# Kernel tuning notes

Measured on AMD Instinct MI355X. Metric: run time of the kernel, lower is better.

Reference implementation:

```python
import jax, jax.numpy as jnp
import numpy as np

_SIGMA = 1.5
_K1 = 0.01
_K2 = 0.03
_WINDOW_SIZE = 11
_N_CHANNELS = 3
_VALUE_RANGE = 1.0
_WEIGHTS = np.array([0.0448, 0.2856, 0.3001, 0.2363, 0.1333], dtype=np.float32)


def create_window(window_size: int, n_channels: int) -> jnp.ndarray:
    # 2D Gaussian kernel, normalized to sum 1, expanded to depthwise (C,1,ws,ws)
    coords = np.arange(window_size, dtype=np.float32) - (window_size - 1) / 2.0
    g = np.exp(-(coords ** 2) / (2.0 * _SIGMA ** 2))
    g = g / g.sum()
    k2d = np.outer(g, g).astype(np.float32)  # (ws, ws), sums to 1
    window = np.broadcast_to(k2d[None, None], (n_channels, 1, window_size, window_size))
    return jnp.asarray(window)


def _dwconv(x, window):
    # depthwise valid conv, NCHW / OIHW
    c = x.shape[1]
    return jax.lax.conv_general_dilated(
        x, window, window_strides=(1, 1), padding='VALID',
        dimension_numbers=('NCHW', 'OIHW', 'NCHW'), feature_group_count=c)


def _avg_pool2(x):
    # torch F.avg_pool2d(kernel=2, stride=2, padding=(H%2, W%2), count_include_pad=True)
    ph = x.shape[-2] % 2
    pw = x.shape[-1] % 2
    s = jax.lax.reduce_window(
        x, 0.0, jax.lax.add, window_dimensions=(1, 1, 2, 2),
        window_strides=(1, 1, 2, 2), padding=((0, 0), (0, 0), (ph, ph), (pw, pw)))
    return s * 0.25


def ssim_per_channel(x, y, window, value_range):
    mu_x = _dwconv(x, window)
    mu_y = _dwconv(y, window)
    mu_x_sq = mu_x ** 2
    mu_y_sq = mu_y ** 2
    mu_xy = mu_x * mu_y
    sigma_x_sq = _dwconv(x * x, window) - mu_x_sq
    sigma_y_sq = _dwconv(y * y, window) - mu_y_sq
    sigma_xy = _dwconv(x * y, window) - mu_xy
    c1 = (_K1 * value_range) ** 2
    c2 = (_K2 * value_range) ** 2
    cs_map = (2.0 * sigma_xy + c2) / (sigma_x_sq + sigma_y_sq + c2)
    ssim_map = (2.0 * mu_xy + c1) / (mu_x_sq + mu_y_sq + c1) * cs_map
    return ssim_map.mean(axis=(-1, -2)), cs_map.mean(axis=(-1, -2))  # (N, C) each


def msssim_per_channel(x, y, window, weights, value_range):
    n_scales = weights.shape[0]
    mcs = []
    for i in range(n_scales):
        if i > 0:
            x = _avg_pool2(x)
            y = _avg_pool2(y)
        ssim_val, cs = ssim_per_channel(x, y, window, value_range)
        mcs.append(jax.nn.relu(cs))
    stacked = jnp.stack(mcs[:-1] + [ssim_val], axis=0)  # (M, N, C)
    stacked = stacked ** weights[:, None, None]
    return jnp.prod(stacked, axis=0)  # (N, C)


def setup_inputs() -> dict:
    key = jax.random.key(0)
    k1, k2 = jax.random.split(key)
    N, C, H, W = 16, 3, 512, 512
    x = jax.random.uniform(k1, (N, C, H, W), dtype=jnp.float32)
    # target correlated with input (realistic distorted-image pair)
    noise = jax.random.uniform(k2, (N, C, H, W), dtype=jnp.float32)
    y = jnp.clip(0.9 * x + 0.1 * noise, 0.0, 1.0)
    window = create_window(_WINDOW_SIZE, _N_CHANNELS)
    weights = jnp.asarray(_WEIGHTS)
    return {"x": x, "y": y, "window": window, "weights": weights}


def reference(x, y, window, weights):
    l = msssim_per_channel(x, y, window, weights, _VALUE_RANGE).mean(axis=-1)  # (N,)
    return l.mean()  # reduction='mean' -> scalar
```

## Files before the change

kernel.cpp:

```cpp
#include <hip/hip_runtime.h>

#define HALO 10
#define NPAIR 76

typedef float v2f __attribute__((ext_vector_type(2)));

#define G0 0.00102838f
#define G1 0.00759871f
#define G2 0.03600077f
#define G3 0.10936069f
#define G4 0.21300556f
#define G5 0.26601176f
#define G6 G4
#define G7 G3
#define G8 G2
#define G9 G1
#define G10 G0

#define HTAP(Q, GW)  { hm += (Q) * (GW); hs += ((Q) * (Q)) * (GW); }

__global__ __launch_bounds__(256, 3) void ssim_wave_kernel(
    const float* __restrict__ x, const float* __restrict__ y,
    float* __restrict__ xo, float* __restrict__ yo,
    float* __restrict__ acc, int H, int W, int ROWS, int do_pool)
{
    const int OH = H - HALO, OW = W - HALO;
    const int nc = blockIdx.z;
    const int tid = threadIdx.x;
    const int wave = tid >> 6, lane = tid & 63;
    const int col0 = blockIdx.x * 64;
    const int r0 = (blockIdx.y * 4 + wave) * ROWS;

    const int c = col0 + lane;
    const bool colvalid = (c < OW);
    const int cl = min(c, W - 1);
    const int chalo = min(col0 + 64 + lane, W - 1);

    const int n_out = min(ROWS, OH - r0);
    const int poolrows = do_pool ? min(ROWS, H - r0) : 0;
    const int n_iter = max(n_out > 0 ? n_out + HALO : 0, poolrows);

    const float* xp = x + (size_t)nc * H * W;
    const float* yp = y + (size_t)nc * H * W;

    __shared__ v2f sUD[4][NPAIR];
    v2f* myUD = sUD[wave];

    v2f Hm0={0.f,0.f}, Hm1=Hm0, Hm2=Hm0, Hm3=Hm0, Hm4=Hm0, Hm5=Hm0,
        Hm6=Hm0, Hm7=Hm0, Hm8=Hm0, Hm9=Hm0, Hm10=Hm0;
    v2f Hs0=Hm0, Hs1=Hm0, Hs2=Hm0, Hs3=Hm0, Hs4=Hm0, Hs5=Hm0,
        Hs6=Hm0, Hs7=Hm0, Hs8=Hm0, Hs9=Hm0, Hs10=Hm0;

    float ssim_sum = 0.f, cs_sum = 0.f;

    float ax = 0.f, ay = 0.f, ahx = 0.f, ahy = 0.f;
    float bx = 0.f, by = 0.f, bhx = 0.f, bhy = 0.f;
    float prevx = 0.f, prevy = 0.f;

    const int Wo = W >> 1;
    float* xop = xo + (size_t)nc * (H >> 1) * Wo + (col0 >> 1);
    float* yop = yo + (size_t)nc * (H >> 1) * Wo + (col0 >> 1);
    const int par = lane & 1;

    if (n_iter > 0) {
        {
            const float* rx = xp + (size_t)r0 * W;
            const float* ry = yp + (size_t)r0 * W;
            ax = rx[cl]; ay = ry[cl];
            if (lane < HALO) { ahx = rx[chalo]; ahy = ry[chalo]; }
            const int r1 = min(r0 + 1, H - 1);
            const float* rx1 = xp + (size_t)r1 * W;
            const float* ry1 = yp + (size_t)r1 * W;
            bx = rx1[cl]; by = ry1[cl];
            if (lane < HALO) { bhx = rx1[chalo]; bhy = ry1[chalo]; }
        }
        const int NI = ((n_iter + 10) / 11) * 11;
        for (int ii = 0; ii < NI; ii += 11) {
#pragma unroll
            for (int u = 0; u < 11; ++u) {
                const int i = ii + u;

                if (do_pool && i < poolrows) {
                    float sx2 = ax + __shfl_xor(ax, 1, 64);
                    float sy2 = ay + __shfl_xor(ay, 1, 64);
                    if (i & 1) {
                        if (par == 0) {
                            const int pr = (r0 + i) >> 1;
                            xop[(size_t)pr * Wo + (lane >> 1)] = 0.25f * (prevx + sx2);
                            yop[(size_t)pr * Wo + (lane >> 1)] = 0.25f * (prevy + sy2);
                        }
                    } else { prevx = sx2; prevy = sy2; }
                }

                {
                    v2f ud; ud.x = ax + ay; ud.y = ax - ay;
                    myUD[lane] = ud;
                    if (lane < HALO) {
                        v2f hh; hh.x = ahx + ahy; hh.y = ahx - ahy;
                        myUD[64 + lane] = hh;
                    }
                }

                {
                    const int rr = min(r0 + i + 2, H - 1);
                    const float* rx = xp + (size_t)rr * W;
                    const float* ry = yp + (size_t)rr * W;
                    ax = rx[cl]; ay = ry[cl];
                    if (lane < HALO) { ahx = rx[chalo]; ahy = ry[chalo]; }
                }

                const v2f* pq = myUD + lane;
                const v2f q0 = pq[0], q1 = pq[1], q2 = pq[2], q3 = pq[3],
                          q4 = pq[4], q5 = pq[5], q6 = pq[6], q7 = pq[7],
                          q8 = pq[8], q9 = pq[9], q10 = pq[10];
                v2f hm = {0.f, 0.f}, hs = {0.f, 0.f};
                HTAP(q0, G0)  HTAP(q1, G1)  HTAP(q2, G2)  HTAP(q3, G3)
                HTAP(q4, G4)  HTAP(q5, G5)  HTAP(q6, G6)  HTAP(q7, G7)
                HTAP(q8, G8)  HTAP(q9, G9)  HTAP(q10, G10)

                Hm0=Hm1; Hm1=Hm2; Hm2=Hm3; Hm3=Hm4; Hm4=Hm5; Hm5=Hm6;
                Hm6=Hm7; Hm7=Hm8; Hm8=Hm9; Hm9=Hm10; Hm10=hm;
                Hs0=Hs1; Hs1=Hs2; Hs2=Hs3; Hs3=Hs4; Hs4=Hs5; Hs5=Hs6;
                Hs6=Hs7; Hs7=Hs8; Hs8=Hs9; Hs9=Hs10; Hs10=hs;

                const int o = i - HALO;
                if (o >= 0 && o < n_out && colvalid) {
                    v2f vm = Hm0*G0; vm += Hm1*G1; vm += Hm2*G2; vm += Hm3*G3;
                    vm += Hm4*G4; vm += Hm5*G5; vm += Hm6*G6; vm += Hm7*G7;
                    vm += Hm8*G8; vm += Hm9*G9; vm += Hm10*G10;
                    v2f vs = Hs0*G0; vs += Hs1*G1; vs += Hs2*G2; vs += Hs3*G3;
                    vs += Hs4*G4; vs += Hs5*G5; vs += Hs6*G6; vs += Hs7*G7;
                    vs += Hs8*G8; vs += Hs9*G9; vs += Hs10*G10;

                    const float A = vm.x, B = vm.y;
                    const float a2 = A * A, b2 = B * B;
                    const float mu_xy = 0.25f * (a2 - b2);
                    const float msum  = 0.5f  * (a2 + b2);
                    const float sig_s  = 0.5f  * (vs.x + vs.y) - msum;
                    const float sig_xy = 0.25f * (vs.x - vs.y) - mu_xy;
                    const float c1 = 1e-4f, c2 = 9e-4f;
                    const float cs = (2.f * sig_xy + c2) * __builtin_amdgcn_rcpf(sig_s + c2);
                    const float ssim = (2.f * mu_xy + c1) * __builtin_amdgcn_rcpf(msum + c1) * cs;
                    ssim_sum += ssim;
                    cs_sum += cs;
                }

                {
                    float t;
                    t = ax;  ax = bx;   bx = t;
                    t = ay;  ay = by;   by = t;
                    t = ahx; ahx = bhx; bhx = t;
                    t = ahy; ahy = bhy; bhy = t;
                }
            }
        }
    }

#pragma unroll
    for (int off = 32; off > 0; off >>= 1) {
        ssim_sum += __shfl_down(ssim_sum, off, 64);
        cs_sum   += __shfl_down(cs_sum,   off, 64);
    }
    if (lane == 0) {
        atomicAdd(&acc[nc * 2 + 0], ssim_sum);
        atomicAdd(&acc[nc * 2 + 1], cs_sum);
    }
}

__global__ void finalize_kernel(const float* __restrict__ acc,
                                const float* __restrict__ weights,
                                float* __restrict__ out)
{
    int t = threadIdx.x;
    float v = 0.f;
    if (t < 48) {
        float prod = 1.f;
#pragma unroll
        for (int s = 0; s < 5; ++s) {
            int O = (512 >> s) - HALO;
            float inv = 1.f / ((float)O * (float)O);
            float ssim = acc[s * 96 + t * 2 + 0] * inv;
            float cs   = acc[s * 96 + t * 2 + 1] * inv;
            float val = (s < 4) ? fmaxf(cs, 0.f) : ssim;
            prod *= powf(val, weights[s]);
        }
        v = prod;
    }
#pragma unroll
    for (int off = 32; off > 0; off >>= 1) v += __shfl_down(v, off, 64);
    if (t == 0) out[0] = v * (1.f / 48.f);
}

extern "C" void kernel_launch(void* const* d_in, const int* in_sizes, int n_in,
                              void* d_out, int out_size, void* d_ws, size_t ws_size,
                              hipStream_t stream) {
    const float* x = (const float*)d_in[0];
    const float* y = (const float*)d_in[1];
    const float* weights = (const float*)d_in[3];
    float* out = (float*)d_out;
    float* ws = (float*)d_ws;

    float* acc = ws;
    float* xs1 = ws + 512;
    float* ys1 = xs1 + (size_t)48 * 256 * 256;
    float* xs2 = ys1 + (size_t)48 * 256 * 256;
    float* ys2 = xs2 + (size_t)48 * 128 * 128;
    float* xs3 = ys2 + (size_t)48 * 128 * 128;
    float* ys3 = xs3 + (size_t)48 * 64 * 64;
    float* xs4 = ys3 + (size_t)48 * 64 * 64;
    float* ys4 = xs4 + (size_t)48 * 32 * 32;

    hipMemsetAsync(acc, 0, 480 * sizeof(float), stream);

    dim3 blk(256);
    ssim_wave_kernel<<<dim3(8, 2, 48), blk, 0, stream>>>(x, y, xs1, ys1, acc + 0 * 96, 512, 512, 64, 1);
    ssim_wave_kernel<<<dim3(4, 2, 48), blk, 0, stream>>>(xs1, ys1, xs2, ys2, acc + 1 * 96, 256, 256, 32, 1);
    ssim_wave_kernel<<<dim3(2, 2, 48), blk, 0, stream>>>(xs2, ys2, xs3, ys3, acc + 2 * 96, 128, 128, 16, 1);
    ssim_wave_kernel<<<dim3(1, 2, 48), blk, 0, stream>>>(xs3, ys3, xs4, ys4, acc + 3 * 96, 64, 64, 8, 1);
    ssim_wave_kernel<<<dim3(1, 1, 48), blk, 0, stream>>>(xs4, ys4, nullptr, nullptr, acc + 4 * 96, 32, 32, 8, 0);

    finalize_kernel<<<dim3(1), dim3(64), 0, stream>>>(acc, weights, out);
}
```

Measured before the change: 256.9 us.

## Double-buffer LDS row staging, prefetch three rows ahead, retune per-scale grid splits

The per-wave LDS row buffer is split into two alternating buffers. Each iteration now reads the previous row's taps before writing the next row, which removes the write-then-read dependency within an iteration, and global loads are issued three rows ahead instead of two. The loop is unrolled by 12, matching a three-register rotation, and exits early instead of running padded iterations. The rows-per-wave and grid shapes for scales 2, 4 and 5 are also retuned. In exchange, LDS use doubles and register pressure rises, and the changed row splits alter the halo-recompute overhead and the number of blocks.

```diff
diff --git a/kernel.cpp b/kernel.cpp
--- a/kernel.cpp
+++ b/kernel.cpp
@@ -19,6 +19,76 @@
 
 #define HTAP(Q, GW)  { hm += (Q) * (GW); hs += ((Q) * (Q)) * (GW); }
 
+
+#define LOADROW(RR, AX, AY, HX, HY)                                  \
+    { const float* rx_ = xp + (size_t)(RR) * W;                      \
+      const float* ry_ = yp + (size_t)(RR) * W;                      \
+      AX = rx_[cl]; AY = ry_[cl];                                    \
+      if (lane < HALO) { HX = rx_[chalo]; HY = ry_[chalo]; } }
+
+#define ITER(U, PAX, PAY, PHX, PHY, SAX, SAY, SHX, SHY)              \
+  {                                                                  \
+    const int i = ii + (U);                                          \
+    if (i >= n_iter) break;                                          \
+     \
+    const v2f* pq = (((U) & 1) ? sB : sA) + lane;                    \
+    const v2f q0 = pq[0], q1 = pq[1], q2 = pq[2], q3 = pq[3],        \
+              q4 = pq[4], q5 = pq[5], q6 = pq[6], q7 = pq[7],        \
+              q8 = pq[8], q9 = pq[9], q10 = pq[10];                  \
+            \
+    if (do_pool && i < poolrows) {                                   \
+        float sx2 = PAX + __shfl_xor(PAX, 1, 64);                    \
+        float sy2 = PAY + __shfl_xor(PAY, 1, 64);                    \
+        if (i & 1) {                                                 \
+            if (par == 0) {                                          \
+                const int pr = (r0 + i) >> 1;                        \
+                xop[(size_t)pr * Wo + (lane >> 1)] = 0.25f * (prevx + sx2); \
+                yop[(size_t)pr * Wo + (lane >> 1)] = 0.25f * (prevy + sy2); \
+            }                                                        \
+        } else { prevx = sx2; prevy = sy2; }                         \
+    }                                                                \
+      \
+    { v2f ud_; ud_.x = SAX + SAY; ud_.y = SAX - SAY;                 \
+      (((U) & 1) ? sA : sB)[lane] = ud_;                             \
+      if (lane < HALO) {                                             \
+          v2f hh_; hh_.x = SHX + SHY; hh_.y = SHX - SHY;             \
+          (((U) & 1) ? sA : sB)[64 + lane] = hh_; } }                \
+          \
+    { const int rr_ = min(r0 + i + 3, H - 1);                        \
+      LOADROW(rr_, PAX, PAY, PHX, PHY) }                             \
+                    \
+    v2f hm = {0.f, 0.f}, hs = {0.f, 0.f};                            \
+    HTAP(q0, G0)  HTAP(q1, G1)  HTAP(q2, G2)  HTAP(q3, G3)           \
+    HTAP(q4, G4)  HTAP(q5, G5)  HTAP(q6, G6)  HTAP(q7, G7)           \
+    HTAP(q8, G8)  HTAP(q9, G9)  HTAP(q10, G10)                       \
+     \
+    Hm0=Hm1; Hm1=Hm2; Hm2=Hm3; Hm3=Hm4; Hm4=Hm5; Hm5=Hm6;           \
+    Hm6=Hm7; Hm7=Hm8; Hm8=Hm9; Hm9=Hm10; Hm10=hm;                   \
+    Hs0=Hs1; Hs1=Hs2; Hs2=Hs3; Hs3=Hs4; Hs4=Hs5; Hs5=Hs6;           \
+    Hs6=Hs7; Hs7=Hs8; Hs8=Hs9; Hs9=Hs10; Hs10=hs;                   \
+                                         \
+    const int o = i - HALO;                                          \
+    if (o >= 0 && o < n_out && colvalid) {                           \
+        v2f vm = Hm0*G0; vm += Hm1*G1; vm += Hm2*G2; vm += Hm3*G3;   \
+        vm += Hm4*G4; vm += Hm5*G5; vm += Hm6*G6; vm += Hm7*G7;      \
+        vm += Hm8*G8; vm += Hm9*G9; vm += Hm10*G10;                  \
+        v2f vs = Hs0*G0; vs += Hs1*G1; vs += Hs2*G2; vs += Hs3*G3;   \
+        vs += Hs4*G4; vs += Hs5*G5; vs += Hs6*G6; vs += Hs7*G7;      \
+        vs += Hs8*G8; vs += Hs9*G9; vs += Hs10*G10;                  \
+        const float A = vm.x, B = vm.y;                              \
+        const float a2 = A * A, b2 = B * B;                          \
+        const float mu_xy = 0.25f * (a2 - b2);                       \
+        const float msum  = 0.5f  * (a2 + b2);                       \
+        const float sig_s  = 0.5f  * (vs.x + vs.y) - msum;           \
+        const float sig_xy = 0.25f * (vs.x - vs.y) - mu_xy;          \
+        const float c1 = 1e-4f, c2 = 9e-4f;                          \
+        const float cs = (2.f * sig_xy + c2) * __builtin_amdgcn_rcpf(sig_s + c2); \
+        const float ssim = (2.f * mu_xy + c1) * __builtin_amdgcn_rcpf(msum + c1) * cs; \
+        ssim_sum += ssim;                                            \
+        cs_sum += cs;                                                \
+    }                                                                \
+  }
+
 __global__ __launch_bounds__(256, 3) void ssim_wave_kernel(
     const float* __restrict__ x, const float* __restrict__ y,
     float* __restrict__ xo, float* __restrict__ yo,
@@ -43,8 +113,9 @@
     const float* xp = x + (size_t)nc * H * W;
     const float* yp = y + (size_t)nc * H * W;
 
-    __shared__ v2f sUD[4][NPAIR];
-    v2f* myUD = sUD[wave];
+    __shared__ v2f sUD[4][2][NPAIR];
+    v2f* sA = sUD[wave][0];
+    v2f* sB = sUD[wave][1];
 
     v2f Hm0={0.f,0.f}, Hm1=Hm0, Hm2=Hm0, Hm3=Hm0, Hm4=Hm0, Hm5=Hm0,
         Hm6=Hm0, Hm7=Hm0, Hm8=Hm0, Hm9=Hm0, Hm10=Hm0;
@@ -53,8 +124,9 @@
 
     float ssim_sum = 0.f, cs_sum = 0.f;
 
-    float ax = 0.f, ay = 0.f, ahx = 0.f, ahy = 0.f;
-    float bx = 0.f, by = 0.f, bhx = 0.f, bhy = 0.f;
+    float ax0=0.f, ay0=0.f, ahx0=0.f, ahy0=0.f;
+    float ax1=0.f, ay1=0.f, ahx1=0.f, ahy1=0.f;
+    float ax2=0.f, ay2=0.f, ahx2=0.f, ahy2=0.f;
     float prevx = 0.f, prevy = 0.f;
 
     const int Wo = W >> 1;
@@ -63,96 +135,27 @@
     const int par = lane & 1;
 
     if (n_iter > 0) {
-        {
-            const float* rx = xp + (size_t)r0 * W;
-            const float* ry = yp + (size_t)r0 * W;
-            ax = rx[cl]; ay = ry[cl];
-            if (lane < HALO) { ahx = rx[chalo]; ahy = ry[chalo]; }
-            const int r1 = min(r0 + 1, H - 1);
-            const float* rx1 = xp + (size_t)r1 * W;
-            const float* ry1 = yp + (size_t)r1 * W;
-            bx = rx1[cl]; by = ry1[cl];
-            if (lane < HALO) { bhx = rx1[chalo]; bhy = ry1[chalo]; }
-        }
-        const int NI = ((n_iter + 10) / 11) * 11;
-        for (int ii = 0; ii < NI; ii += 11) {
-#pragma unroll
-            for (int u = 0; u < 11; ++u) {
-                const int i = ii + u;
-
-                if (do_pool && i < poolrows) {
-                    float sx2 = ax + __shfl_xor(ax, 1, 64);
-                    float sy2 = ay + __shfl_xor(ay, 1, 64);
-                    if (i & 1) {
-                        if (par == 0) {
-                            const int pr = (r0 + i) >> 1;
-                            xop[(size_t)pr * Wo + (lane >> 1)] = 0.25f * (prevx + sx2);
-                            yop[(size_t)pr * Wo + (lane >> 1)] = 0.25f * (prevy + sy2);
-                        }
-                    } else { prevx = sx2; prevy = sy2; }
-                }
-
-                {
-                    v2f ud; ud.x = ax + ay; ud.y = ax - ay;
-                    myUD[lane] = ud;
-                    if (lane < HALO) {
-                        v2f hh; hh.x = ahx + ahy; hh.y = ahx - ahy;
-                        myUD[64 + lane] = hh;
-                    }
-                }
-
-                {
-                    const int rr = min(r0 + i + 2, H - 1);
-                    const float* rx = xp + (size_t)rr * W;
-                    const float* ry = yp + (size_t)rr * W;
-                    ax = rx[cl]; ay = ry[cl];
-                    if (lane < HALO) { ahx = rx[chalo]; ahy = ry[chalo]; }
-                }
-
-                const v2f* pq = myUD + lane;
-                const v2f q0 = pq[0], q1 = pq[1], q2 = pq[2], q3 = pq[3],
-                          q4 = pq[4], q5 = pq[5], q6 = pq[6], q7 = pq[7],
-                          q8 = pq[8], q9 = pq[9], q10 = pq[10];
-                v2f hm = {0.f, 0.f}, hs = {0.f, 0.f};
-                HTAP(q0, G0)  HTAP(q1, G1)  HTAP(q2, G2)  HTAP(q3, G3)
-                HTAP(q4, G4)  HTAP(q5, G5)  HTAP(q6, G6)  HTAP(q7, G7)
-                HTAP(q8, G8)  HTAP(q9, G9)  HTAP(q10, G10)
-
-                Hm0=Hm1; Hm1=Hm2; Hm2=Hm3; Hm3=Hm4; Hm4=Hm5; Hm5=Hm6;
-                Hm6=Hm7; Hm7=Hm8; Hm8=Hm9; Hm9=Hm10; Hm10=hm;
-                Hs0=Hs1; Hs1=Hs2; Hs2=Hs3; Hs3=Hs4; Hs4=Hs5; Hs5=Hs6;
-                Hs6=Hs7; Hs7=Hs8; Hs8=Hs9; Hs9=Hs10; Hs10=hs;
-
-                const int o = i - HALO;
-                if (o >= 0 && o < n_out && colvalid) {
-                    v2f vm = Hm0*G0; vm += Hm1*G1; vm += Hm2*G2; vm += Hm3*G3;
-                    vm += Hm4*G4; vm += Hm5*G5; vm += Hm6*G6; vm += Hm7*G7;
-                    vm += Hm8*G8; vm += Hm9*G9; vm += Hm10*G10;
-                    v2f vs = Hs0*G0; vs += Hs1*G1; vs += Hs2*G2; vs += Hs3*G3;
-                    vs += Hs4*G4; vs += Hs5*G5; vs += Hs6*G6; vs += Hs7*G7;
-                    vs += Hs8*G8; vs += Hs9*G9; vs += Hs10*G10;
-
-                    const float A = vm.x, B = vm.y;
-                    const float a2 = A * A, b2 = B * B;
-                    const float mu_xy = 0.25f * (a2 - b2);
-                    const float msum  = 0.5f  * (a2 + b2);
-                    const float sig_s  = 0.5f  * (vs.x + vs.y) - msum;
-                    const float sig_xy = 0.25f * (vs.x - vs.y) - mu_xy;
-                    const float c1 = 1e-4f, c2 = 9e-4f;
-                    const float cs = (2.f * sig_xy + c2) * __builtin_amdgcn_rcpf(sig_s + c2);
-                    const float ssim = (2.f * mu_xy + c1) * __builtin_amdgcn_rcpf(msum + c1) * cs;
-                    ssim_sum += ssim;
-                    cs_sum += cs;
-                }
-
-                {
-                    float t;
-                    t = ax;  ax = bx;   bx = t;
-                    t = ay;  ay = by;   by = t;
-                    t = ahx; ahx = bhx; bhx = t;
-                    t = ahy; ahy = bhy; bhy = t;
-                }
-            }
+        LOADROW(r0, ax0, ay0, ahx0, ahy0)
+        { const int r1_ = min(r0 + 1, H - 1); LOADROW(r1_, ax1, ay1, ahx1, ahy1) }
+        { const int r2_ = min(r0 + 2, H - 1); LOADROW(r2_, ax2, ay2, ahx2, ahy2) }
+        { v2f ud_; ud_.x = ax0 + ay0; ud_.y = ax0 - ay0; sA[lane] = ud_;
+          if (lane < HALO) {
+              v2f hh_; hh_.x = ahx0 + ahy0; hh_.y = ahx0 - ahy0;
+              sA[64 + lane] = hh_; } }
+
+        for (int ii = 0; ii < n_iter; ii += 12) {
+            ITER(0,  ax0, ay0, ahx0, ahy0,  ax1, ay1, ahx1, ahy1)
+            ITER(1,  ax1, ay1, ahx1, ahy1,  ax2, ay2, ahx2, ahy2)
+            ITER(2,  ax2, ay2, ahx2, ahy2,  ax0, ay0, ahx0, ahy0)
+            ITER(3,  ax0, ay0, ahx0, ahy0,  ax1, ay1, ahx1, ahy1)
+            ITER(4,  ax1, ay1, ahx1, ahy1,  ax2, ay2, ahx2, ahy2)
+            ITER(5,  ax2, ay2, ahx2, ahy2,  ax0, ay0, ahx0, ahy0)
+            ITER(6,  ax0, ay0, ahx0, ahy0,  ax1, ay1, ahx1, ahy1)
+            ITER(7,  ax1, ay1, ahx1, ahy1,  ax2, ay2, ahx2, ahy2)
+            ITER(8,  ax2, ay2, ahx2, ahy2,  ax0, ay0, ahx0, ahy0)
+            ITER(9,  ax0, ay0, ahx0, ahy0,  ax1, ay1, ahx1, ahy1)
+            ITER(10, ax1, ay1, ahx1, ahy1,  ax2, ay2, ahx2, ahy2)
+            ITER(11, ax2, ay2, ahx2, ahy2,  ax0, ay0, ahx0, ahy0)
         }
     }
 
@@ -214,10 +217,10 @@
 
     dim3 blk(256);
     ssim_wave_kernel<<<dim3(8, 2, 48), blk, 0, stream>>>(x, y, xs1, ys1, acc + 0 * 96, 512, 512, 64, 1);
-    ssim_wave_kernel<<<dim3(4, 2, 48), blk, 0, stream>>>(xs1, ys1, xs2, ys2, acc + 1 * 96, 256, 256, 32, 1);
+    ssim_wave_kernel<<<dim3(4, 1, 48), blk, 0, stream>>>(xs1, ys1, xs2, ys2, acc + 1 * 96, 256, 256, 64, 1);
     ssim_wave_kernel<<<dim3(2, 2, 48), blk, 0, stream>>>(xs2, ys2, xs3, ys3, acc + 2 * 96, 128, 128, 16, 1);
-    ssim_wave_kernel<<<dim3(1, 2, 48), blk, 0, stream>>>(xs3, ys3, xs4, ys4, acc + 3 * 96, 64, 64, 8, 1);
-    ssim_wave_kernel<<<dim3(1, 1, 48), blk, 0, stream>>>(xs4, ys4, nullptr, nullptr, acc + 4 * 96, 32, 32, 8, 0);
+    ssim_wave_kernel<<<dim3(1, 4, 48), blk, 0, stream>>>(xs3, ys3, xs4, ys4, acc + 3 * 96, 64, 64, 4, 1);
+    ssim_wave_kernel<<<dim3(1, 2, 48), blk, 0, stream>>>(xs4, ys4, nullptr, nullptr, acc + 4 * 96, 32, 32, 4, 0);
 
     finalize_kernel<<<dim3(1), dim3(64), 0, stream>>>(acc, weights, out);
 }
```

After: 272.6 us. 1.06x slower.
